# Optimization experiments

Measured on AMD Instinct MI355X. Metric: run time of the kernel, lower is better.

The kernel has to match this reference:

```python
import jax, jax.numpy as jnp
import numpy as np
from jax import lax

B, S, H, E, P, K, R = 64, 512, 768, 32, 16, 9, 6
HEADS, C1, C2 = 4, 128, 64
FEAT = 4 * C2 + 1  # e1, e2, e1*e2, context (64 each) + log-distance


def _ln(x, g, b):
    m = x.mean(-1, keepdims=True)
    v = ((x - m) ** 2).mean(-1, keepdims=True)
    return (x - m) * lax.rsqrt(v + 1e-5) * g + b


def _gat(x, adj, W, a_s, a_d, bias, heads, cout, concat):
    # Dense GATConv over a small fully-masked entity graph. adj[b,i,j]=edge j->i (incl. self-loops).
    h = jnp.einsum('bef,fhc->behc', x, W.reshape(x.shape[-1], heads, cout))
    s = jnp.einsum('behc,hc->bhe', h, a_s)  # source-node attention term
    d = jnp.einsum('behc,hc->bhe', h, a_d)  # target-node attention term
    logits = jax.nn.leaky_relu(d[:, :, :, None] + s[:, :, None, :], 0.2)  # [b,h,i,j]
    logits = jnp.where(adj[:, None, :, :], logits, -1e9)
    att = jax.nn.softmax(logits, axis=-1)
    out = jnp.einsum('bhij,bjhc->bihc', att, h)
    out = out.reshape(out.shape[0], out.shape[1], heads * cout) if concat else out.mean(2)
    return out + bias


def _crf_nll(em, tags, mask, start, end, trans):
    # torchcrf: loss = -mean log-likelihood. em [B,S,K]; tags [B,S]; mask [B,S] bool.
    emt = jnp.transpose(em, (1, 0, 2))
    tgt = tags.T
    mkt = mask.T.astype(em.dtype)
    num0 = start[tgt[0]] + jnp.take_along_axis(emt[0], tgt[0][:, None], 1)[:, 0]

    def nstep(c, inp):
        ptag, sc = c
        e, t, m = inp
        step = trans[ptag, t] + jnp.take_along_axis(e, t[:, None], 1)[:, 0]
        return (jnp.where(m > 0, t, ptag), sc + step * m), None

    (ltag, num), _ = lax.scan(nstep, (tgt[0], num0), (emt[1:], tgt[1:], mkt[1:]))
    num = num + end[ltag]
    a0 = start[None, :] + emt[0]

    def dstep(a, inp):
        e, m = inp
        nxt = jax.scipy.special.logsumexp(a[:, :, None] + trans[None] + e[:, None, :], axis=1)
        return jnp.where(m[:, None] > 0, nxt, a), None

    aT, _ = lax.scan(dstep, a0, (emt[1:], mkt[1:]))
    Z = jax.scipy.special.logsumexp(aT + end[None], axis=1)
    return jnp.mean(Z - num)


def setup_inputs() -> dict:
    key = jax.random.key(0)
    ks = jax.random.split(key, 24)
    n = lambda i, shape, s=0.05: jax.random.normal(ks[i], shape, jnp.float32) * s
    return {
        'sequence_output': jax.random.normal(ks[0], (B, S, H), jnp.float32),
        'attention_mask': jnp.ones((B, S), jnp.int32),
        'ner_labels': jax.random.randint(ks[1], (B, S), 0, K),
        'entity_start': jax.random.randint(ks[2], (B, E), 0, S - 8),
        'entity_len': jax.random.randint(ks[3], (B, E), 0, 8),
        'pair_e1': jax.random.randint(ks[4], (B, P), 0, E),
        'pair_e2': jax.random.randint(ks[5], (B, P), 0, E),
        'pair_labels': jax.random.randint(ks[6], (B, P), 0, 2),
        'adj_mask': jnp.ones((B, E, E), bool),
        'w_ner1': n(7, (H, 256)), 'b_ner1': jnp.zeros((256,), jnp.float32),
        'w_ner2': n(8, (256, K)), 'b_ner2': jnp.zeros((K,), jnp.float32),
        'crf_start': n(9, (K,), 0.1), 'crf_end': n(10, (K,), 0.1), 'crf_trans': n(11, (K, K), 0.1),
        'w_gat1': n(12, (H, HEADS * C1)), 'a_src1': n(13, (HEADS, C1)), 'a_dst1': n(14, (HEADS, C1)),
        'b_gat1': jnp.zeros((HEADS * C1,), jnp.float32),
        'w_gat2': n(15, (HEADS * C1, C2)), 'a_src2': n(16, (1, C2)), 'a_dst2': n(17, (1, C2)),
        'b_gat2': jnp.zeros((C2,), jnp.float32),
        'w_fe': n(18, (FEAT, 512)), 'b_fe': jnp.zeros((512,), jnp.float32),
        'g_fe': jnp.ones((512,), jnp.float32), 'be_fe': jnp.zeros((512,), jnp.float32),
        'w_rc1': n(19, (R, 512, 256)), 'b_rc1': jnp.zeros((R, 256), jnp.float32),
        'g_rc': jnp.ones((R, 256), jnp.float32), 'be_rc': jnp.zeros((R, 256), jnp.float32),
        'w_rc2': n(20, (R, 256, 1)), 'b_rc2': jnp.zeros((R,), jnp.float32),
    }


def reference(sequence_output, attention_mask, ner_labels, entity_start, entity_len,
              pair_e1, pair_e2, pair_labels, adj_mask,
              w_ner1, b_ner1, w_ner2, b_ner2, crf_start, crf_end, crf_trans,
              w_gat1, a_src1, a_dst1, b_gat1, w_gat2, a_src2, a_dst2, b_gat2,
              w_fe, b_fe, g_fe, be_fe, w_rc1, b_rc1, g_rc, be_rc, w_rc2, b_rc2):
    # NER head (dropout off / eval)
    ner_logits = jnp.maximum(sequence_output @ w_ner1 + b_ner1, 0.0) @ w_ner2 + b_ner2
    ner_loss = _crf_nll(ner_logits, ner_labels, attention_mask.astype(bool),
                        crf_start, crf_end, crf_trans)
    # entity span mean-pool via inclusive cumsum trick
    cs = jnp.concatenate([jnp.zeros((B, 1, H), sequence_output.dtype),
                          jnp.cumsum(sequence_output, axis=1)], axis=1)
    e_end = jnp.clip(entity_start + entity_len, 0, S - 1)
    seg = (jnp.take_along_axis(cs, (e_end + 1)[:, :, None], 1)
           - jnp.take_along_axis(cs, entity_start[:, :, None], 1))
    ent = seg / (e_end - entity_start + 1).astype(sequence_output.dtype)[:, :, None]  # [B,E,H]
    x = _gat(ent, adj_mask, w_gat1, a_src1, a_dst1, b_gat1, HEADS, C1, True)
    x = jnp.maximum(x, 0.0)
    x = _gat(x, adj_mask, w_gat2, a_src2, a_dst2, b_gat2, 1, C2, False)  # [B,E,64]
    x1 = jnp.take_along_axis(x, pair_e1[:, :, None], 1)
    x2 = jnp.take_along_axis(x, pair_e2[:, :, None], 1)
    ctx = jnp.broadcast_to(x.mean(1, keepdims=True), (B, P, C2))
    dist = jnp.log(jnp.abs(pair_e1 - pair_e2).astype(x.dtype) + 1.0)[:, :, None]
    pf = jnp.concatenate([x1, x2, x1 * x2, ctx, dist], axis=-1)  # [B,P,257]
    fe = jax.nn.leaky_relu(_ln(pf @ w_fe + b_fe, g_fe, be_fe), 0.01)
    h1 = jnp.einsum('bpf,rfo->rbpo', fe, w_rc1) + b_rc1[:, None, None, :]
    h1 = jax.nn.leaky_relu(_ln(h1, g_rc[:, None, None, :], be_rc[:, None, None, :]), 0.01)
    z = jnp.einsum('rbpo,ro->rbp', h1, w_rc2[:, :, 0]) + b_rc2[:, None, None]
    y = pair_labels.astype(z.dtype)[None]
    # BCEWithLogitsLoss(pos_weight=2.0), mean per relation type, summed over types
    bce = -(2.0 * y * jax.nn.log_sigmoid(z) + (1.0 - y) * jax.nn.log_sigmoid(-z))
    rel_loss = bce.mean(axis=(1, 2)).sum()
    total = ner_loss + rel_loss
    return ner_logits, z, total
```

## Files before the change

### kernel.cpp

```cpp
#include <hip/hip_runtime.h>
#include <math.h>


#define NB 64
#define NS 512
#define NH 768
#define NE 32
#define NP 16
#define NK 9
#define NR 6
#define NHEADS 4
#define NC1 128
#define NC2 64
#define SEGS 16
#define SEGLEN 32

#define ZOFF 294912
#define TOTOFF 301056

#define WS_ENT   0u
#define WS_HG1   1572864u
#define WS_X1    2621440u
#define WS_H2    3670016u
#define WS_X2    3801088u
#define WS_S1    3932160u
#define WS_D1    3940352u
#define WS_S2    3948544u
#define WS_D2    3950592u
#define WS_CTX   3952640u
#define WS_PF    3956736u
#define WS_FE    4222976u
#define WS_CRF   4747264u
#define WS_REL   4747328u
#define WS_W1T   4747392u
#define WS_WRT   0u
#define WS_WFET  393216u
#define WS_SEG   475136u

typedef __attribute__((ext_vector_type(8))) short bf16x8;
typedef __attribute__((ext_vector_type(4))) float f32x4;

__device__ __forceinline__ unsigned short f2bf(float x) {
  union { float f; unsigned u; } v; v.f = x;
  unsigned r = v.u + 0x7FFFu + ((v.u >> 16) & 1u);
  return (unsigned short)(r >> 16);
}

__device__ __forceinline__ float logsigf(float x) {
  if (x >= 0.f) return -log1pf(__expf(-x));
  return x - log1pf(__expf(x));
}

__global__ __launch_bounds__(256) void k_w1t(const float* __restrict__ w1,
    unsigned short* __restrict__ w1t) {
  const int k = blockIdx.x, t = threadIdx.x;
  w1t[t * NH + k] = f2bf(w1[k * 256 + t]);
}

__global__ __launch_bounds__(256) void k_wrt(const float* __restrict__ w1,
    unsigned short* __restrict__ wrt) {
  __shared__ unsigned short tr[256 * 72];
  const int r = blockIdx.x >> 3, kt = blockIdx.x & 7;
  const int k0 = kt * 64, t = threadIdx.x;
#pragma unroll
  for (int i = 0; i < 16; i++) {
    const int slot = t + 256 * i;
    const int row = slot >> 6, c4 = slot & 63;
    const float4 f = *reinterpret_cast<const float4*>(
        &w1[((size_t)(r * 512) + k0 + row) * 256 + c4 * 4]);
    tr[(c4 * 4 + 0) * 72 + row] = f2bf(f.x);
    tr[(c4 * 4 + 1) * 72 + row] = f2bf(f.y);
    tr[(c4 * 4 + 2) * 72 + row] = f2bf(f.z);
    tr[(c4 * 4 + 3) * 72 + row] = f2bf(f.w);
  }
  __syncthreads();
#pragma unroll
  for (int i = 0; i < 8; i++) {
    const int slot = t + 256 * i;
    const int col = slot >> 3, q = slot & 7;
    *reinterpret_cast<uint4*>(&wrt[((size_t)(r * 256 + col)) * 512 + k0 + q * 8]) =
        *reinterpret_cast<const uint4*>(&tr[col * 72 + q * 8]);
  }
}

__global__ __launch_bounds__(256) void k_wfet(const float* __restrict__ w,
    unsigned short* __restrict__ wt) {
  __shared__ unsigned short tr[256 * 72];
  const int kt = blockIdx.x % 5, cb = blockIdx.x / 5;
  const int k0 = kt * 64, c0 = cb * 256, t = threadIdx.x;
#pragma unroll
  for (int i = 0; i < 16; i++) {
    const int slot = t + 256 * i;
    const int row = slot >> 6, c4 = slot & 63;
    const int k = k0 + row;
    float4 f = {0.f, 0.f, 0.f, 0.f};
    if (k < 257)
      f = *reinterpret_cast<const float4*>(&w[(size_t)k * 512 + c0 + c4 * 4]);
    tr[(c4 * 4 + 0) * 72 + row] = f2bf(f.x);
    tr[(c4 * 4 + 1) * 72 + row] = f2bf(f.y);
    tr[(c4 * 4 + 2) * 72 + row] = f2bf(f.z);
    tr[(c4 * 4 + 3) * 72 + row] = f2bf(f.w);
  }
  __syncthreads();
#pragma unroll
  for (int i = 0; i < 8; i++) {
    const int slot = t + 256 * i;
    const int col = slot >> 3, q = slot & 7;
    *reinterpret_cast<uint4*>(&wt[((size_t)(c0 + col)) * 320 + k0 + q * 8]) =
        *reinterpret_cast<const uint4*>(&tr[col * 72 + q * 8]);
  }
}

__global__ __launch_bounds__(256) void k_ner(const float* __restrict__ seq,
    const unsigned short* __restrict__ w1t, const float* __restrict__ b1,
    const float* __restrict__ w2, const float* __restrict__ b2,
    float* __restrict__ out) {
  __shared__ unsigned short AsS[64 * 40];
  __shared__ unsigned short BsS[256 * 40];
  __shared__ float zs[64 * 4 * 12];
  const int t = threadIdx.x;
  const int tok0 = blockIdx.x * 64;
  const int w = t >> 6, lane = t & 63, quad = lane >> 4, l15 = lane & 15;

  f32x4 acc[4][4];
#pragma unroll
  for (int r = 0; r < 4; r++)
#pragma unroll
    for (int c = 0; c < 4; c++) acc[r][c] = (f32x4){0.f, 0.f, 0.f, 0.f};

  const int tokA = t >> 2, koffA = (t & 3) * 8;
  const float* aptr = seq + (size_t)(tok0 + tokA) * NH + koffA;

  for (int kt = 0; kt < NH; kt += 32) {
    __syncthreads();
    {
      const float4 f0 = *reinterpret_cast<const float4*>(aptr + kt);
      const float4 f1 = *reinterpret_cast<const float4*>(aptr + kt + 4);
      bf16x8 av;
      av[0] = (short)f2bf(f0.x); av[1] = (short)f2bf(f0.y);
      av[2] = (short)f2bf(f0.z); av[3] = (short)f2bf(f0.w);
      av[4] = (short)f2bf(f1.x); av[5] = (short)f2bf(f1.y);
      av[6] = (short)f2bf(f1.z); av[7] = (short)f2bf(f1.w);
      *reinterpret_cast<bf16x8*>(&AsS[tokA * 40 + koffA]) = av;
    }
#pragma unroll
    for (int i = 0; i < 4; i++) {
      const int q = t + 256 * i;
      const int col = q >> 2, koff = (q & 3) * 8;
      *reinterpret_cast<uint4*>(&BsS[col * 40 + koff]) =
          *reinterpret_cast<const uint4*>(&w1t[(size_t)col * NH + kt + koff]);
    }
    __syncthreads();
    bf16x8 a[4], b[4];
#pragma unroll
    for (int r = 0; r < 4; r++)
      a[r] = *reinterpret_cast<const bf16x8*>(&AsS[(r * 16 + l15) * 40 + quad * 8]);
#pragma unroll
    for (int c = 0; c < 4; c++)
      b[c] = *reinterpret_cast<const bf16x8*>(&BsS[(w * 64 + c * 16 + l15) * 40 + quad * 8]);
#pragma unroll
    for (int r = 0; r < 4; r++)
#pragma unroll
      for (int c = 0; c < 4; c++)
        acc[r][c] = __builtin_amdgcn_mfma_f32_16x16x32_bf16(a[r], b[c], acc[r][c], 0, 0, 0);
  }

  float b1v[4], w2v[4][NK];
#pragma unroll
  for (int c = 0; c < 4; c++) {
    const int col = w * 64 + c * 16 + l15;
    b1v[c] = b1[col];
#pragma unroll
    for (int cc = 0; cc < NK; cc++) w2v[c][cc] = w2[col * NK + cc];
  }
#pragma unroll
  for (int r = 0; r < 4; r++) {
#pragma unroll
    for (int reg = 0; reg < 4; reg++) {
      float p[NK];
#pragma unroll
      for (int cc = 0; cc < NK; cc++) p[cc] = 0.f;
#pragma unroll
      for (int c = 0; c < 4; c++) {
        const float h = fmaxf(acc[r][c][reg] + b1v[c], 0.f);
#pragma unroll
        for (int cc = 0; cc < NK; cc++) p[cc] = fmaf(h, w2v[c][cc], p[cc]);
      }
#pragma unroll
      for (int o = 1; o < 16; o <<= 1)
#pragma unroll
        for (int cc = 0; cc < NK; cc++) p[cc] += __shfl_xor(p[cc], o);
      if (l15 == 0) {
        const int tokr = r * 16 + quad * 4 + reg;
#pragma unroll
        for (int cc = 0; cc < NK; cc++) zs[(tokr * 4 + w) * 12 + cc] = p[cc];
      }
    }
  }
  __syncthreads();
  if (t < 64) {
#pragma unroll
    for (int cc = 0; cc < NK; cc++) {
      const float z = zs[(t * 4 + 0) * 12 + cc] + zs[(t * 4 + 1) * 12 + cc] +
                      zs[(t * 4 + 2) * 12 + cc] + zs[(t * 4 + 3) * 12 + cc] + b2[cc];
      out[(size_t)(tok0 + t) * NK + cc] = z;
    }
  }
}

__global__ __launch_bounds__(128) void k_crf_seg(const float* __restrict__ em,
    const int* __restrict__ mask, const float* __restrict__ trans,
    float* __restrict__ segm) {
  __shared__ float bufA[16 * 81];
  __shared__ float bufB[8 * 81];
  __shared__ float ems[SEGLEN * 9];
  __shared__ int mks[SEGLEN];
  __shared__ float trs[81];
  const int blk = blockIdx.x;
  const int b = blk >> 4, seg = blk & 15;
  const int t = threadIdx.x;
  const int s0 = 1 + seg * SEGLEN;
  const float* emb = em + (size_t)b * NS * NK;
  const int* mk = mask + b * NS;
  if (t < 81) trs[t] = trans[t];
  for (int i = t; i < SEGLEN * 9; i += 128) {
    const int g = s0 * 9 + i;
    ems[i] = (g < NS * 9) ? emb[g] : 0.f;
  }
  if (t < SEGLEN) {
    const int s = s0 + t;
    mks[t] = (s < NS) ? mk[s] : 0;
  }
  __syncthreads();
  for (int idx = t; idx < 16 * 81; idx += 128) {
    const int p = idx / 81, e = idx % 81, i = e / 9, j = e % 9;
    const int la = 2 * p, lb = la + 1;
    const bool ma = mks[la] > 0, mb = mks[lb] > 0;
    float r;
    if (ma && mb) {
      float v[9], mx = -1e30f;
#pragma unroll
      for (int m = 0; m < 9; m++) {
        v[m] = trs[i * 9 + m] + ems[la * 9 + m] + trs[m * 9 + j];
        mx = fmaxf(mx, v[m]);
      }
      float sum = 0.f;
#pragma unroll
      for (int m = 0; m < 9; m++) sum += __expf(v[m] - mx);
      r = mx + __logf(sum) + ems[lb * 9 + j];
    } else if (ma) {
      r = trs[e] + ems[la * 9 + j];
    } else if (mb) {
      r = trs[e] + ems[lb * 9 + j];
    } else {
      r = (i == j) ? 0.f : -1e30f;
    }
    bufA[p * 81 + e] = r;
  }
  float* src = bufA;
  float* dst = bufB;
  for (int n = 16; n > 1; n >>= 1) {
    __syncthreads();
    const int half = n >> 1;
    for (int idx = t; idx < half * 81; idx += 128) {
      const int q = idx / 81, e = idx % 81, i = e / 9, j = e % 9;
      const float* A = src + (size_t)(2 * q) * 81;
      const float* Bm = src + (size_t)(2 * q + 1) * 81;
      float v[9], mx = -1e30f;
#pragma unroll
      for (int m = 0; m < 9; m++) {
        v[m] = A[i * 9 + m] + Bm[m * 9 + j];
        mx = fmaxf(mx, v[m]);
      }
      float sum = 0.f;
#pragma unroll
      for (int m = 0; m < 9; m++) sum += __expf(v[m] - mx);
      dst[q * 81 + e] = mx + __logf(sum);
    }
    float* tmp = src; src = dst; dst = tmp;
  }
  __syncthreads();
  if (t < 81) segm[((size_t)b * SEGS + seg) * 81 + t] = src[t];
}

__global__ __launch_bounds__(64) void k_crf_fin(const float* __restrict__ em,
    const int* __restrict__ tags, const int* __restrict__ mask,
    const float* __restrict__ startv, const float* __restrict__ endv,
    const float* __restrict__ trans, const float* __restrict__ segm,
    float* __restrict__ lossb) {
  __shared__ float sm[SEGS * 81];
  __shared__ float av[16];
  __shared__ float red[2];
  const int b = blockIdx.x, t = threadIdx.x;
  const float* emb = em + (size_t)b * NS * NK;
  const int* mk = mask + b * NS;
  const int* tg = tags + b * NS;
  for (int i = t; i < SEGS * 81; i += 64) sm[i] = segm[(size_t)b * SEGS * 81 + i];
  {
    float num = 0.f;
    int lastS = 0;
#pragma unroll
    for (int o = 0; o < 8; o++) {
      const int s = t * 8 + o;
      if (s >= 1 && mk[s] > 0) {
        const int cur = tg[s], prv = tg[s - 1];
        num += trans[prv * NK + cur] + emb[s * NK + cur];
        lastS = s;
      }
    }
#pragma unroll
    for (int o = 32; o > 0; o >>= 1) {
      num += __shfl_xor(num, o);
      lastS = max(lastS, __shfl_xor(lastS, o));
    }
    if (t == 0) {
      const int t0 = tg[0];
      red[0] = startv[t0] + emb[t0] + num + endv[tg[lastS]];
    }
  }
  __syncthreads();
  if (t < 9) av[t] = startv[t] + emb[t];
  __syncthreads();
  for (int h = 0; h < SEGS; h++) {
    float nv = 0.f;
    if (t < 9) {
      float v[9], mx = -1e30f;
#pragma unroll
      for (int i2 = 0; i2 < 9; i2++) {
        v[i2] = av[i2] + sm[h * 81 + i2 * 9 + t];
        mx = fmaxf(mx, v[i2]);
      }
      float sum = 0.f;
#pragma unroll
      for (int i2 = 0; i2 < 9; i2++) sum += __expf(v[i2] - mx);
      nv = mx + __logf(sum);
    }
    __syncthreads();
    if (t < 9) av[t] = nv;
    __syncthreads();
  }
  if (t == 0) {
    float mx = -1e30f;
#pragma unroll
    for (int j = 0; j < 9; j++) mx = fmaxf(mx, av[j] + endv[j]);
    float sum = 0.f;
#pragma unroll
    for (int j = 0; j < 9; j++) sum += __expf(av[j] + endv[j] - mx);
    lossb[b] = (mx + __logf(sum)) - red[0];
  }
}

__global__ __launch_bounds__(256) void k_ent(const float* __restrict__ seq,
    const int* __restrict__ est, const int* __restrict__ elen, float* __restrict__ ent) {
  const int be = blockIdx.x;
  const int b = be >> 5, e = be & 31;
  const int st = est[b * NE + e];
  int en = st + elen[b * NE + e];
  en = min(max(en, 0), NS - 1);
  const float inv = 1.f / (float)(en - st + 1);
  for (int c = threadIdx.x; c < NH; c += 256) {
    float s = 0.f;
    for (int r = st; r <= en; r++) s += seq[((size_t)b * NS + r) * NH + c];
    ent[((size_t)b * NE + e) * NH + c] = s * inv;
  }
}

__global__ __launch_bounds__(256) void k_g1(const float* __restrict__ ent,
    const float* __restrict__ w, float* __restrict__ hout) {
  __shared__ float As[32 * 36];
  __shared__ float Bs[32 * 128];
  const int b = blockIdx.x >> 2, cb = blockIdx.x & 3;
  const int t = threadIdx.x;
  const int tc = t & 31, tr = t >> 5;
  float acc[4][4];
#pragma unroll
  for (int i = 0; i < 4; i++)
#pragma unroll
    for (int j = 0; j < 4; j++) acc[i][j] = 0.f;
  for (int kt = 0; kt < NH; kt += 32) {
    __syncthreads();
    {
      const int e = t >> 3, k4 = t & 7;
      *reinterpret_cast<float4*>(&As[e * 36 + k4 * 4]) =
          *reinterpret_cast<const float4*>(&ent[((size_t)b * NE + e) * NH + kt + k4 * 4]);
    }
#pragma unroll
    for (int i = 0; i < 4; i++) {
      const int slot = t + 256 * i;
      const int row = slot >> 5, cg = slot & 31;
      *reinterpret_cast<float4*>(&Bs[row * 128 + cg * 4]) =
          *reinterpret_cast<const float4*>(&w[(size_t)(kt + row) * 512 + cb * 128 + cg * 4]);
    }
    __syncthreads();
#pragma unroll
    for (int kg = 0; kg < 8; kg++) {
      float4 a[4];
#pragma unroll
      for (int i = 0; i < 4; i++)
        a[i] = *reinterpret_cast<const float4*>(&As[(tr * 4 + i) * 36 + kg * 4]);
#pragma unroll
      for (int k2 = 0; k2 < 4; k2++) {
        const float4 bv = *reinterpret_cast<const float4*>(&Bs[(kg * 4 + k2) * 128 + tc * 4]);
#pragma unroll
        for (int i = 0; i < 4; i++) {
          const float av = reinterpret_cast<const float*>(&a[i])[k2];
          acc[i][0] = fmaf(av, bv.x, acc[i][0]);
          acc[i][1] = fmaf(av, bv.y, acc[i][1]);
          acc[i][2] = fmaf(av, bv.z, acc[i][2]);
          acc[i][3] = fmaf(av, bv.w, acc[i][3]);
        }
      }
    }
  }
#pragma unroll
  for (int i = 0; i < 4; i++) {
    float4 v;
    v.x = acc[i][0]; v.y = acc[i][1]; v.z = acc[i][2]; v.w = acc[i][3];
    *reinterpret_cast<float4*>(&hout[((size_t)b * NE + tr * 4 + i) * 512 + cb * 128 + tc * 4]) = v;
  }
}

__global__ __launch_bounds__(128) void k_sd1(const float* __restrict__ h,
    const float* __restrict__ as, const float* __restrict__ ad,
    float* __restrict__ s1, float* __restrict__ d1) {
  __shared__ float sm[4];
  const int be = blockIdx.x;
  const int b = be >> 5, e = be & 31;
  const int t = threadIdx.x;
  for (int hd = 0; hd < NHEADS; hd++) {
    const float v = h[((size_t)b * NE + e) * 512 + hd * NC1 + t];
    float sv = v * as[hd * NC1 + t];
    float dv = v * ad[hd * NC1 + t];
#pragma unroll
    for (int o = 32; o > 0; o >>= 1) { sv += __shfl_xor(sv, o); dv += __shfl_xor(dv, o); }
    if ((t & 63) == 0) { sm[(t >> 6) * 2] = sv; sm[(t >> 6) * 2 + 1] = dv; }
    __syncthreads();
    if (t == 0) {
      s1[(b * NHEADS + hd) * NE + e] = sm[0] + sm[2];
      d1[(b * NHEADS + hd) * NE + e] = sm[1] + sm[3];
    }
    __syncthreads();
  }
}

__global__ __launch_bounds__(128) void k_att1(const float* __restrict__ h,
    const float* __restrict__ s1, const float* __restrict__ d1,
    const unsigned char* __restrict__ adj, const float* __restrict__ bias,
    float* __restrict__ x1) {
  __shared__ float att[NE];
  const int blk = blockIdx.x;
  const int i = blk & 31, hd = (blk >> 5) & 3, b = blk >> 7;
  const int t = threadIdx.x;
  if (t < NE) {
    float lg = d1[(b * NHEADS + hd) * NE + i] + s1[(b * NHEADS + hd) * NE + t];
    lg = lg >= 0.f ? lg : 0.2f * lg;
    if (!adj[((size_t)b * NE + i) * NE + t]) lg = -1e9f;
    att[t] = lg;
  }
  __syncthreads();
  if (t == 0) {
    float m = -1e30f;
#pragma unroll
    for (int j = 0; j < NE; j++) m = fmaxf(m, att[j]);
    float ex[NE];
    float sum = 0.f;
#pragma unroll
    for (int j = 0; j < NE; j++) { ex[j] = __expf(att[j] - m); sum += ex[j]; }
    const float inv = 1.f / sum;
#pragma unroll
    for (int j = 0; j < NE; j++) att[j] = ex[j] * inv;
  }
  __syncthreads();
  float acc = bias[hd * NC1 + t];
  for (int j = 0; j < NE; j++)
    acc += att[j] * h[((size_t)b * NE + j) * 512 + hd * NC1 + t];
  x1[((size_t)b * NE + i) * 512 + hd * NC1 + t] = fmaxf(acc, 0.f);
}

__global__ __launch_bounds__(256) void k_g2(const float* __restrict__ x1,
    const float* __restrict__ w, const float* __restrict__ as, const float* __restrict__ ad,
    float* __restrict__ h2, float* __restrict__ s2, float* __restrict__ d2) {
  __shared__ float As[32 * 36];
  __shared__ float Bs[32 * 64];
  const int b = blockIdx.x;
  const int t = threadIdx.x;
  const int tc = t & 15, tr = t >> 4;
  float acc[2][4];
#pragma unroll
  for (int i = 0; i < 2; i++)
#pragma unroll
    for (int j = 0; j < 4; j++) acc[i][j] = 0.f;
  for (int kt = 0; kt < 512; kt += 32) {
    __syncthreads();
    {
      const int e = t >> 3, k4 = t & 7;
      *reinterpret_cast<float4*>(&As[e * 36 + k4 * 4]) =
          *reinterpret_cast<const float4*>(&x1[((size_t)b * NE + e) * 512 + kt + k4 * 4]);
    }
#pragma unroll
    for (int i = 0; i < 2; i++) {
      const int slot = t + 256 * i;
      const int row = slot >> 4, cg = slot & 15;
      *reinterpret_cast<float4*>(&Bs[row * 64 + cg * 4]) =
          *reinterpret_cast<const float4*>(&w[(size_t)(kt + row) * NC2 + cg * 4]);
    }
    __syncthreads();
#pragma unroll
    for (int kg = 0; kg < 8; kg++) {
      float4 a[2];
#pragma unroll
      for (int i = 0; i < 2; i++)
        a[i] = *reinterpret_cast<const float4*>(&As[(tr * 2 + i) * 36 + kg * 4]);
#pragma unroll
      for (int k2 = 0; k2 < 4; k2++) {
        const float4 bv = *reinterpret_cast<const float4*>(&Bs[(kg * 4 + k2) * 64 + tc * 4]);
#pragma unroll
        for (int i = 0; i < 2; i++) {
          const float av = reinterpret_cast<const float*>(&a[i])[k2];
          acc[i][0] = fmaf(av, bv.x, acc[i][0]);
          acc[i][1] = fmaf(av, bv.y, acc[i][1]);
          acc[i][2] = fmaf(av, bv.z, acc[i][2]);
          acc[i][3] = fmaf(av, bv.w, acc[i][3]);
        }
      }
    }
  }
  const float4 a4s = *reinterpret_cast<const float4*>(&as[tc * 4]);
  const float4 a4d = *reinterpret_cast<const float4*>(&ad[tc * 4]);
#pragma unroll
  for (int i = 0; i < 2; i++) {
    const int e = tr * 2 + i;
    float4 v;
    v.x = acc[i][0]; v.y = acc[i][1]; v.z = acc[i][2]; v.w = acc[i][3];
    *reinterpret_cast<float4*>(&h2[((size_t)b * NE + e) * NC2 + tc * 4]) = v;
    float sv = v.x * a4s.x + v.y * a4s.y + v.z * a4s.z + v.w * a4s.w;
    float dv = v.x * a4d.x + v.y * a4d.y + v.z * a4d.z + v.w * a4d.w;
#pragma unroll
    for (int o = 8; o > 0; o >>= 1) { sv += __shfl_xor(sv, o); dv += __shfl_xor(dv, o); }
    if (tc == 0) { s2[b * NE + e] = sv; d2[b * NE + e] = dv; }
  }
}

__global__ __launch_bounds__(64) void k_att2(const float* __restrict__ h2,
    const float* __restrict__ s2, const float* __restrict__ d2,
    const unsigned char* __restrict__ adj, const float* __restrict__ bias,
    float* __restrict__ x2) {
  __shared__ float att[NE];
  const int be = blockIdx.x;
  const int b = be >> 5, i = be & 31;
  const int t = threadIdx.x;
  if (t < NE) {
    float lg = d2[b * NE + i] + s2[b * NE + t];
    lg = lg >= 0.f ? lg : 0.2f * lg;
    if (!adj[((size_t)b * NE + i) * NE + t]) lg = -1e9f;
    att[t] = lg;
  }
  __syncthreads();
  if (t == 0) {
    float m = -1e30f;
#pragma unroll
    for (int j = 0; j < NE; j++) m = fmaxf(m, att[j]);
    float ex[NE];
    float sum = 0.f;
#pragma unroll
    for (int j = 0; j < NE; j++) { ex[j] = __expf(att[j] - m); sum += ex[j]; }
    const float inv = 1.f / sum;
#pragma unroll
    for (int j = 0; j < NE; j++) att[j] = ex[j] * inv;
  }
  __syncthreads();
  float acc = bias[t];
  for (int j = 0; j < NE; j++)
    acc += att[j] * h2[((size_t)b * NE + j) * NC2 + t];
  x2[((size_t)b * NE + i) * NC2 + t] = acc;
}

__global__ __launch_bounds__(64) void k_ctx(const float* __restrict__ x2, float* __restrict__ ctx) {
  const int b = blockIdx.x, t = threadIdx.x;
  float s = 0.f;
  for (int e = 0; e < NE; e++) s += x2[((size_t)b * NE + e) * NC2 + t];
  ctx[b * NC2 + t] = s * (1.f / NE);
}

__global__ __launch_bounds__(64) void k_pf(const float* __restrict__ x2,
    const float* __restrict__ ctx, const int* __restrict__ pe1, const int* __restrict__ pe2,
    float* __restrict__ pf) {
  const int bp = blockIdx.x;
  const int b = bp >> 4, p = bp & 15;
  const int t = threadIdx.x;
  const int e1 = pe1[b * NP + p], e2 = pe2[b * NP + p];
  const float v1 = x2[((size_t)b * NE + e1) * NC2 + t];
  const float v2 = x2[((size_t)b * NE + e2) * NC2 + t];
  float* row = pf + (size_t)bp * 260;
  row[t] = v1;
  row[64 + t] = v2;
  row[128 + t] = v1 * v2;
  row[192 + t] = ctx[b * NC2 + t];
  if (t == 0) row[256] = logf(fabsf((float)(e1 - e2)) + 1.f);
  if (t < 3) row[257 + t] = 0.f;
}

__global__ __launch_bounds__(256) void k_fe(const float* __restrict__ pf,
    const unsigned short* __restrict__ wt, const float* __restrict__ bfe,
    const float* __restrict__ g, const float* __restrict__ be,
    unsigned short* __restrict__ feb) {
  __shared__ unsigned short Af[16 * 320];
  __shared__ float Cs[16 * 520];
  const int b = blockIdx.x, t = threadIdx.x;
  const int w = t >> 6, lane = t & 63, quad = lane >> 4, l15 = lane & 15;
  for (int i = t; i < 16 * 320; i += 256) {
    const int p = i / 320, k = i - p * 320;
    Af[i] = (k < 260) ? f2bf(pf[(size_t)(b * NP + p) * 260 + k]) : (unsigned short)0;
  }
  __syncthreads();
  f32x4 acc[8];
#pragma unroll
  for (int c = 0; c < 8; c++) acc[c] = (f32x4){0.f, 0.f, 0.f, 0.f};
#pragma unroll
  for (int kt = 0; kt < 10; kt++) {
    const bf16x8 a = *reinterpret_cast<const bf16x8*>(&Af[l15 * 320 + kt * 32 + quad * 8]);
#pragma unroll
    for (int c = 0; c < 8; c++) {
      const int col = w * 128 + c * 16 + l15;
      const bf16x8 bv = *reinterpret_cast<const bf16x8*>(&wt[(size_t)col * 320 + kt * 32 + quad * 8]);
      acc[c] = __builtin_amdgcn_mfma_f32_16x16x32_bf16(a, bv, acc[c], 0, 0, 0);
    }
  }
#pragma unroll
  for (int c = 0; c < 8; c++)
#pragma unroll
    for (int reg = 0; reg < 4; reg++)
      Cs[(quad * 4 + reg) * 520 + w * 128 + c * 16 + l15] = acc[c][reg];
  __syncthreads();
  float bfev[8], gv[8], bev[8];
#pragma unroll
  for (int ch = 0; ch < 8; ch++) {
    const int col = ch * 64 + lane;
    bfev[ch] = bfe[col]; gv[ch] = g[col]; bev[ch] = be[col];
  }
#pragma unroll
  for (int pp = 0; pp < 4; pp++) {
    const int p = w * 4 + pp;
    float v[8], s = 0.f, sq = 0.f;
#pragma unroll
    for (int ch = 0; ch < 8; ch++) {
      v[ch] = Cs[p * 520 + ch * 64 + lane] + bfev[ch];
      s += v[ch]; sq += v[ch] * v[ch];
    }
#pragma unroll
    for (int o = 32; o > 0; o >>= 1) { s += __shfl_xor(s, o); sq += __shfl_xor(sq, o); }
    const float mean = s * (1.f / 512.f);
    const float var = sq * (1.f / 512.f) - mean * mean;
    const float rr = rsqrtf(var + 1e-5f);
#pragma unroll
    for (int ch = 0; ch < 8; ch++) {
      float n = (v[ch] - mean) * rr * gv[ch] + bev[ch];
      n = n >= 0.f ? n : 0.01f * n;
      feb[(size_t)(b * NP + p) * 512 + ch * 64 + lane] = f2bf(n);
    }
  }
}

__global__ __launch_bounds__(256) void k_rc(const unsigned short* __restrict__ feb,
    const unsigned short* __restrict__ wrt, const float* __restrict__ b1,
    const float* __restrict__ g, const float* __restrict__ be,
    const float* __restrict__ w2, const float* __restrict__ b2,
    const int* __restrict__ ylab, float* __restrict__ zout, float* __restrict__ relacc) {
  __shared__ unsigned short Af[16 * 520];
  __shared__ float Cs[16 * 264];
  const int blk = blockIdx.x;
  const int r = blk >> 6, b = blk & 63;
  const int t = threadIdx.x;
  const int w = t >> 6, lane = t & 63, quad = lane >> 4, l15 = lane & 15;
#pragma unroll
  for (int i = 0; i < 4; i++) {
    const int slot = t + 256 * i;
    const int p = slot >> 6, q = slot & 63;
    *reinterpret_cast<uint4*>(&Af[p * 520 + q * 8]) =
        *reinterpret_cast<const uint4*>(&feb[(size_t)(b * NP + p) * 512 + q * 8]);
  }
  __syncthreads();
  f32x4 acc[4];
#pragma unroll
  for (int c = 0; c < 4; c++) acc[c] = (f32x4){0.f, 0.f, 0.f, 0.f};
#pragma unroll
  for (int kt = 0; kt < 16; kt++) {
    const bf16x8 a = *reinterpret_cast<const bf16x8*>(&Af[l15 * 520 + kt * 32 + quad * 8]);
#pragma unroll
    for (int c = 0; c < 4; c++) {
      const int col = w * 64 + c * 16 + l15;
      const bf16x8 bv = *reinterpret_cast<const bf16x8*>(
          &wrt[(size_t)(r * 256 + col) * 512 + kt * 32 + quad * 8]);
      acc[c] = __builtin_amdgcn_mfma_f32_16x16x32_bf16(a, bv, acc[c], 0, 0, 0);
    }
  }
#pragma unroll
  for (int c = 0; c < 4; c++)
#pragma unroll
    for (int reg = 0; reg < 4; reg++)
      Cs[(quad * 4 + reg) * 264 + w * 64 + c * 16 + l15] = acc[c][reg];
  __syncthreads();
  float b1v[4], gv[4], bev[4], w2v[4];
#pragma unroll
  for (int ch = 0; ch < 4; ch++) {
    const int col = r * 256 + ch * 64 + lane;
    b1v[ch] = b1[col]; gv[ch] = g[col]; bev[ch] = be[col]; w2v[ch] = w2[col];
  }
  const float b2v = b2[r];
  float local = 0.f;
#pragma unroll
  for (int pp = 0; pp < 4; pp++) {
    const int p = w * 4 + pp;
    float v[4], s = 0.f, sq = 0.f;
#pragma unroll
    for (int ch = 0; ch < 4; ch++) {
      v[ch] = Cs[p * 264 + ch * 64 + lane] + b1v[ch];
      s += v[ch]; sq += v[ch] * v[ch];
    }
#pragma unroll
    for (int o = 32; o > 0; o >>= 1) { s += __shfl_xor(s, o); sq += __shfl_xor(sq, o); }
    const float mean = s * (1.f / 256.f);
    const float var = sq * (1.f / 256.f) - mean * mean;
    const float rr = rsqrtf(var + 1e-5f);
    float zdot = 0.f;
#pragma unroll
    for (int ch = 0; ch < 4; ch++) {
      float n = (v[ch] - mean) * rr * gv[ch] + bev[ch];
      n = n >= 0.f ? n : 0.01f * n;
      zdot = fmaf(n, w2v[ch], zdot);
    }
#pragma unroll
    for (int o = 32; o > 0; o >>= 1) zdot += __shfl_xor(zdot, o);
    if (lane == 0) {
      const float zp = zdot + b2v;
      zout[(size_t)(r * NB + b) * NP + p] = zp;
      const float y = (float)ylab[b * NP + p];
      local += -(2.f * y * logsigf(zp) + (1.f - y) * logsigf(-zp));
    }
  }
  if (lane == 0) atomicAdd(relacc, local * (1.f / (NB * NP)));
}

__global__ __launch_bounds__(64) void k_fin(const float* __restrict__ lossb,
    const float* __restrict__ rel, float* __restrict__ out) {
  float v = lossb[threadIdx.x];
#pragma unroll
  for (int o = 32; o > 0; o >>= 1) v += __shfl_down(v, o);
  if (threadIdx.x == 0) out[TOTOFF] = v * (1.f / NB) + rel[0];
}

extern "C" void kernel_launch(void* const* d_in, const int* in_sizes, int n_in,
                              void* d_out, int out_size, void* d_ws, size_t ws_size,
                              hipStream_t stream) {
  const float* seq = (const float*)d_in[0];
  const int* amask = (const int*)d_in[1];
  const int* nlab = (const int*)d_in[2];
  const int* est = (const int*)d_in[3];
  const int* elen = (const int*)d_in[4];
  const int* pe1 = (const int*)d_in[5];
  const int* pe2 = (const int*)d_in[6];
  const int* plab = (const int*)d_in[7];
  const unsigned char* adj = (const unsigned char*)d_in[8];
  const float* w_ner1 = (const float*)d_in[9];
  const float* b_ner1 = (const float*)d_in[10];
  const float* w_ner2 = (const float*)d_in[11];
  const float* b_ner2 = (const float*)d_in[12];
  const float* crf_start = (const float*)d_in[13];
  const float* crf_end = (const float*)d_in[14];
  const float* crf_trans = (const float*)d_in[15];
  const float* w_gat1 = (const float*)d_in[16];
  const float* a_src1 = (const float*)d_in[17];
  const float* a_dst1 = (const float*)d_in[18];
  const float* b_gat1 = (const float*)d_in[19];
  const float* w_gat2 = (const float*)d_in[20];
  const float* a_src2 = (const float*)d_in[21];
  const float* a_dst2 = (const float*)d_in[22];
  const float* b_gat2 = (const float*)d_in[23];
  const float* w_fe = (const float*)d_in[24];
  const float* b_fe = (const float*)d_in[25];
  const float* g_fe = (const float*)d_in[26];
  const float* be_fe = (const float*)d_in[27];
  const float* w_rc1 = (const float*)d_in[28];
  const float* b_rc1 = (const float*)d_in[29];
  const float* g_rc = (const float*)d_in[30];
  const float* be_rc = (const float*)d_in[31];
  const float* w_rc2 = (const float*)d_in[32];
  const float* b_rc2 = (const float*)d_in[33];

  float* out = (float*)d_out;
  float* ws = (float*)d_ws;
  float* ent = ws + WS_ENT;
  float* hg1 = ws + WS_HG1;
  float* x1 = ws + WS_X1;
  float* h2 = ws + WS_H2;
  float* x2 = ws + WS_X2;
  float* s1 = ws + WS_S1;
  float* d1 = ws + WS_D1;
  float* s2 = ws + WS_S2;
  float* d2 = ws + WS_D2;
  float* ctx = ws + WS_CTX;
  float* pf = ws + WS_PF;
  float* crfb = ws + WS_CRF;
  float* rel = ws + WS_REL;
  unsigned short* w1t = (unsigned short*)(ws + WS_W1T);
  unsigned short* feb = (unsigned short*)(ws + WS_FE);
  unsigned short* wrt = (unsigned short*)(ws + WS_WRT);
  unsigned short* wfet = (unsigned short*)(ws + WS_WFET);
  float* segm = ws + WS_SEG;

  hipMemsetAsync(rel, 0, sizeof(float), stream);

  k_w1t<<<NH, 256, 0, stream>>>(w_ner1, w1t);
  k_ner<<<512, 256, 0, stream>>>(seq, w1t, b_ner1, w_ner2, b_ner2, out);
  k_ent<<<NB * NE, 256, 0, stream>>>(seq, est, elen, ent);
  k_g1<<<NB * 4, 256, 0, stream>>>(ent, w_gat1, hg1);
  k_wrt<<<NR * 8, 256, 0, stream>>>(w_rc1, wrt);
  k_wfet<<<10, 256, 0, stream>>>(w_fe, wfet);
  k_crf_seg<<<NB * SEGS, 128, 0, stream>>>(out, amask, crf_trans, segm);
  k_crf_fin<<<NB, 64, 0, stream>>>(out, nlab, amask, crf_start, crf_end, crf_trans,
                                   segm, crfb);
  k_sd1<<<NB * NE, 128, 0, stream>>>(hg1, a_src1, a_dst1, s1, d1);
  k_att1<<<NB * NHEADS * NE, 128, 0, stream>>>(hg1, s1, d1, adj, b_gat1, x1);
  k_g2<<<NB, 256, 0, stream>>>(x1, w_gat2, a_src2, a_dst2, h2, s2, d2);
  k_att2<<<NB * NE, 64, 0, stream>>>(h2, s2, d2, adj, b_gat2, x2);
  k_ctx<<<NB, 64, 0, stream>>>(x2, ctx);
  k_pf<<<NB * NP, 64, 0, stream>>>(x2, ctx, pe1, pe2, pf);
  k_fe<<<NB, 256, 0, stream>>>(pf, wfet, b_fe, g_fe, be_fe, feb);
  k_rc<<<NR * NB, 256, 0, stream>>>(feb, wrt, b_rc1, g_rc, be_rc, w_rc2, b_rc2,
                                    plab, out + ZOFF, rel);
  k_fin<<<1, 64, 0, stream>>>(crfb, rel, out);
}
```

Measured before the change: 444.1 us.

## Fuse GAT projection, attention scores, softmax and aggregation into per-head kernels

Merges the GAT layer-1 projection with the src/dst score computation, softmax and neighbor aggregation into one kernel per (batch, head), doing the same for layer 2. The context mean is folded into the pair-feature kernel, and the two weight-conversion kernels are merged into one launch. The NER weight transpose now goes through shared memory with coalesced vector stores. This removes several launches and the global round-trips of intermediate h, s, d and ctx buffers. In exchange, the pair kernel redundantly recomputes the entity mean for each pair, and a single warp per block does the softmax.

```diff
diff --git a/kernel.cpp b/kernel.cpp
--- a/kernel.cpp
+++ b/kernel.cpp
@@ -19,15 +19,8 @@
 #define TOTOFF 301056
 
 #define WS_ENT   0u
-#define WS_HG1   1572864u
 #define WS_X1    2621440u
-#define WS_H2    3670016u
 #define WS_X2    3801088u
-#define WS_S1    3932160u
-#define WS_D1    3940352u
-#define WS_S2    3948544u
-#define WS_D2    3950592u
-#define WS_CTX   3952640u
 #define WS_PF    3956736u
 #define WS_FE    4222976u
 #define WS_CRF   4747264u
@@ -53,61 +46,79 @@
 
 __global__ __launch_bounds__(256) void k_w1t(const float* __restrict__ w1,
     unsigned short* __restrict__ w1t) {
-  const int k = blockIdx.x, t = threadIdx.x;
-  w1t[t * NH + k] = f2bf(w1[k * 256 + t]);
-}
-
-__global__ __launch_bounds__(256) void k_wrt(const float* __restrict__ w1,
-    unsigned short* __restrict__ wrt) {
+  __shared__ unsigned short tr[32 * 776];
+  const int c0 = blockIdx.x * 32;
+  const int t = threadIdx.x;
+#pragma unroll
+  for (int p = 0; p < 24; p++) {
+    const int k = p * 32 + (t >> 3), c4 = t & 7;
+    const float4 f = *reinterpret_cast<const float4*>(&w1[(size_t)k * 256 + c0 + c4 * 4]);
+    tr[(c4 * 4 + 0) * 776 + k] = f2bf(f.x);
+    tr[(c4 * 4 + 1) * 776 + k] = f2bf(f.y);
+    tr[(c4 * 4 + 2) * 776 + k] = f2bf(f.z);
+    tr[(c4 * 4 + 3) * 776 + k] = f2bf(f.w);
+  }
+  __syncthreads();
+  const int c = t >> 3, q = t & 7;
+#pragma unroll
+  for (int i = 0; i < 12; i++) {
+    *reinterpret_cast<uint4*>(&w1t[(size_t)(c0 + c) * NH + q * 96 + i * 8]) =
+        *reinterpret_cast<const uint4*>(&tr[c * 776 + q * 96 + i * 8]);
+  }
+}
+
+__global__ __launch_bounds__(256) void k_wconv(const float* __restrict__ wrc,
+    const float* __restrict__ wfe, unsigned short* __restrict__ wrt,
+    unsigned short* __restrict__ wfet) {
   __shared__ unsigned short tr[256 * 72];
-  const int r = blockIdx.x >> 3, kt = blockIdx.x & 7;
-  const int k0 = kt * 64, t = threadIdx.x;
-#pragma unroll
-  for (int i = 0; i < 16; i++) {
-    const int slot = t + 256 * i;
-    const int row = slot >> 6, c4 = slot & 63;
-    const float4 f = *reinterpret_cast<const float4*>(
-        &w1[((size_t)(r * 512) + k0 + row) * 256 + c4 * 4]);
-    tr[(c4 * 4 + 0) * 72 + row] = f2bf(f.x);
-    tr[(c4 * 4 + 1) * 72 + row] = f2bf(f.y);
-    tr[(c4 * 4 + 2) * 72 + row] = f2bf(f.z);
-    tr[(c4 * 4 + 3) * 72 + row] = f2bf(f.w);
-  }
-  __syncthreads();
-#pragma unroll
-  for (int i = 0; i < 8; i++) {
-    const int slot = t + 256 * i;
-    const int col = slot >> 3, q = slot & 7;
-    *reinterpret_cast<uint4*>(&wrt[((size_t)(r * 256 + col)) * 512 + k0 + q * 8]) =
-        *reinterpret_cast<const uint4*>(&tr[col * 72 + q * 8]);
-  }
-}
-
-__global__ __launch_bounds__(256) void k_wfet(const float* __restrict__ w,
-    unsigned short* __restrict__ wt) {
-  __shared__ unsigned short tr[256 * 72];
-  const int kt = blockIdx.x % 5, cb = blockIdx.x / 5;
-  const int k0 = kt * 64, c0 = cb * 256, t = threadIdx.x;
-#pragma unroll
-  for (int i = 0; i < 16; i++) {
-    const int slot = t + 256 * i;
-    const int row = slot >> 6, c4 = slot & 63;
-    const int k = k0 + row;
-    float4 f = {0.f, 0.f, 0.f, 0.f};
-    if (k < 257)
-      f = *reinterpret_cast<const float4*>(&w[(size_t)k * 512 + c0 + c4 * 4]);
-    tr[(c4 * 4 + 0) * 72 + row] = f2bf(f.x);
-    tr[(c4 * 4 + 1) * 72 + row] = f2bf(f.y);
-    tr[(c4 * 4 + 2) * 72 + row] = f2bf(f.z);
-    tr[(c4 * 4 + 3) * 72 + row] = f2bf(f.w);
-  }
-  __syncthreads();
-#pragma unroll
-  for (int i = 0; i < 8; i++) {
-    const int slot = t + 256 * i;
-    const int col = slot >> 3, q = slot & 7;
-    *reinterpret_cast<uint4*>(&wt[((size_t)(c0 + col)) * 320 + k0 + q * 8]) =
-        *reinterpret_cast<const uint4*>(&tr[col * 72 + q * 8]);
+  const int t = threadIdx.x;
+  if (blockIdx.x < 48) {
+    const int r = blockIdx.x >> 3, kt = blockIdx.x & 7;
+    const int k0 = kt * 64;
+#pragma unroll
+    for (int i = 0; i < 16; i++) {
+      const int slot = t + 256 * i;
+      const int row = slot >> 6, c4 = slot & 63;
+      const float4 f = *reinterpret_cast<const float4*>(
+          &wrc[((size_t)(r * 512) + k0 + row) * 256 + c4 * 4]);
+      tr[(c4 * 4 + 0) * 72 + row] = f2bf(f.x);
+      tr[(c4 * 4 + 1) * 72 + row] = f2bf(f.y);
+      tr[(c4 * 4 + 2) * 72 + row] = f2bf(f.z);
+      tr[(c4 * 4 + 3) * 72 + row] = f2bf(f.w);
+    }
+    __syncthreads();
+#pragma unroll
+    for (int i = 0; i < 8; i++) {
+      const int slot = t + 256 * i;
+      const int col = slot >> 3, q = slot & 7;
+      *reinterpret_cast<uint4*>(&wrt[((size_t)(r * 256 + col)) * 512 + k0 + q * 8]) =
+          *reinterpret_cast<const uint4*>(&tr[col * 72 + q * 8]);
+    }
+  } else {
+    const int bid = blockIdx.x - 48;
+    const int kt = bid % 5, cb = bid / 5;
+    const int k0 = kt * 64, c0 = cb * 256;
+#pragma unroll
+    for (int i = 0; i < 16; i++) {
+      const int slot = t + 256 * i;
+      const int row = slot >> 6, c4 = slot & 63;
+      const int k = k0 + row;
+      float4 f = {0.f, 0.f, 0.f, 0.f};
+      if (k < 257)
+        f = *reinterpret_cast<const float4*>(&wfe[(size_t)k * 512 + c0 + c4 * 4]);
+      tr[(c4 * 4 + 0) * 72 + row] = f2bf(f.x);
+      tr[(c4 * 4 + 1) * 72 + row] = f2bf(f.y);
+      tr[(c4 * 4 + 2) * 72 + row] = f2bf(f.z);
+      tr[(c4 * 4 + 3) * 72 + row] = f2bf(f.w);
+    }
+    __syncthreads();
+#pragma unroll
+    for (int i = 0; i < 8; i++) {
+      const int slot = t + 256 * i;
+      const int col = slot >> 3, q = slot & 7;
+      *reinterpret_cast<uint4*>(&wfet[((size_t)(c0 + col)) * 320 + k0 + q * 8]) =
+          *reinterpret_cast<const uint4*>(&tr[col * 72 + q * 8]);
+    }
   }
 }
 
@@ -365,11 +376,16 @@
   }
 }
 
-__global__ __launch_bounds__(256) void k_g1(const float* __restrict__ ent,
-    const float* __restrict__ w, float* __restrict__ hout) {
+__global__ __launch_bounds__(256) void k_g1f(const float* __restrict__ ent,
+    const float* __restrict__ w, const float* __restrict__ as,
+    const float* __restrict__ ad, const unsigned char* __restrict__ adj,
+    const float* __restrict__ bias, float* __restrict__ x1) {
   __shared__ float As[32 * 36];
   __shared__ float Bs[32 * 128];
-  const int b = blockIdx.x >> 2, cb = blockIdx.x & 3;
+  __shared__ float Hs[32 * 132];
+  __shared__ float Att[32 * 32];
+  __shared__ float Sv[32], Dv[32];
+  const int b = blockIdx.x >> 2, hd = blockIdx.x & 3;
   const int t = threadIdx.x;
   const int tc = t & 31, tr = t >> 5;
   float acc[4][4];
@@ -389,7 +405,7 @@
       const int slot = t + 256 * i;
       const int row = slot >> 5, cg = slot & 31;
       *reinterpret_cast<float4*>(&Bs[row * 128 + cg * 4]) =
-          *reinterpret_cast<const float4*>(&w[(size_t)(kt + row) * 512 + cb * 128 + cg * 4]);
+          *reinterpret_cast<const float4*>(&w[(size_t)(kt + row) * 512 + hd * 128 + cg * 4]);
     }
     __syncthreads();
 #pragma unroll
@@ -413,75 +429,76 @@
     }
   }
 #pragma unroll
+  for (int i = 0; i < 4; i++)
+#pragma unroll
+    for (int j = 0; j < 4; j++)
+      Hs[(tr * 4 + i) * 132 + tc * 4 + j] = acc[i][j];
+  __syncthreads();
+  {
+    const int e = t >> 3, cg = t & 7;
+    float sv = 0.f, dv = 0.f;
+#pragma unroll
+    for (int c = 0; c < 16; c++) {
+      const float h = Hs[e * 132 + cg * 16 + c];
+      sv += h * as[hd * NC1 + cg * 16 + c];
+      dv += h * ad[hd * NC1 + cg * 16 + c];
+    }
+#pragma unroll
+    for (int o = 1; o < 8; o <<= 1) { sv += __shfl_xor(sv, o); dv += __shfl_xor(dv, o); }
+    if (cg == 0) { Sv[e] = sv; Dv[e] = dv; }
+  }
+  __syncthreads();
+  if (t < 32) {
+    const int i = t;
+    const float di = Dv[i];
+    float lg[32];
+    float m = -1e30f;
+#pragma unroll
+    for (int j = 0; j < 32; j++) {
+      float v = di + Sv[j];
+      v = v >= 0.f ? v : 0.2f * v;
+      if (!adj[((size_t)b * NE + i) * NE + j]) v = -1e9f;
+      lg[j] = v; m = fmaxf(m, v);
+    }
+    float sum = 0.f;
+#pragma unroll
+    for (int j = 0; j < 32; j++) { lg[j] = __expf(lg[j] - m); sum += lg[j]; }
+    const float inv = 1.f / sum;
+#pragma unroll
+    for (int j = 0; j < 32; j++) Att[j * 32 + i] = lg[j] * inv;
+  }
+  __syncthreads();
+#pragma unroll
   for (int i = 0; i < 4; i++) {
+    const int row = tr * 4 + i;
+    float o0 = bias[hd * NC1 + tc * 4 + 0];
+    float o1 = bias[hd * NC1 + tc * 4 + 1];
+    float o2 = bias[hd * NC1 + tc * 4 + 2];
+    float o3 = bias[hd * NC1 + tc * 4 + 3];
+#pragma unroll
+    for (int j = 0; j < 32; j++) {
+      const float a = Att[j * 32 + row];
+      o0 = fmaf(a, Hs[j * 132 + tc * 4 + 0], o0);
+      o1 = fmaf(a, Hs[j * 132 + tc * 4 + 1], o1);
+      o2 = fmaf(a, Hs[j * 132 + tc * 4 + 2], o2);
+      o3 = fmaf(a, Hs[j * 132 + tc * 4 + 3], o3);
+    }
     float4 v;
-    v.x = acc[i][0]; v.y = acc[i][1]; v.z = acc[i][2]; v.w = acc[i][3];
-    *reinterpret_cast<float4*>(&hout[((size_t)b * NE + tr * 4 + i) * 512 + cb * 128 + tc * 4]) = v;
-  }
-}
-
-__global__ __launch_bounds__(128) void k_sd1(const float* __restrict__ h,
-    const float* __restrict__ as, const float* __restrict__ ad,
-    float* __restrict__ s1, float* __restrict__ d1) {
-  __shared__ float sm[4];
-  const int be = blockIdx.x;
-  const int b = be >> 5, e = be & 31;
-  const int t = threadIdx.x;
-  for (int hd = 0; hd < NHEADS; hd++) {
-    const float v = h[((size_t)b * NE + e) * 512 + hd * NC1 + t];
-    float sv = v * as[hd * NC1 + t];
-    float dv = v * ad[hd * NC1 + t];
-#pragma unroll
-    for (int o = 32; o > 0; o >>= 1) { sv += __shfl_xor(sv, o); dv += __shfl_xor(dv, o); }
-    if ((t & 63) == 0) { sm[(t >> 6) * 2] = sv; sm[(t >> 6) * 2 + 1] = dv; }
-    __syncthreads();
-    if (t == 0) {
-      s1[(b * NHEADS + hd) * NE + e] = sm[0] + sm[2];
-      d1[(b * NHEADS + hd) * NE + e] = sm[1] + sm[3];
-    }
-    __syncthreads();
-  }
-}
-
-__global__ __launch_bounds__(128) void k_att1(const float* __restrict__ h,
-    const float* __restrict__ s1, const float* __restrict__ d1,
-    const unsigned char* __restrict__ adj, const float* __restrict__ bias,
-    float* __restrict__ x1) {
-  __shared__ float att[NE];
-  const int blk = blockIdx.x;
-  const int i = blk & 31, hd = (blk >> 5) & 3, b = blk >> 7;
-  const int t = threadIdx.x;
-  if (t < NE) {
-    float lg = d1[(b * NHEADS + hd) * NE + i] + s1[(b * NHEADS + hd) * NE + t];
-    lg = lg >= 0.f ? lg : 0.2f * lg;
-    if (!adj[((size_t)b * NE + i) * NE + t]) lg = -1e9f;
-    att[t] = lg;
-  }
-  __syncthreads();
-  if (t == 0) {
-    float m = -1e30f;
-#pragma unroll
-    for (int j = 0; j < NE; j++) m = fmaxf(m, att[j]);
-    float ex[NE];
-    float sum = 0.f;
-#pragma unroll
-    for (int j = 0; j < NE; j++) { ex[j] = __expf(att[j] - m); sum += ex[j]; }
-    const float inv = 1.f / sum;
-#pragma unroll
-    for (int j = 0; j < NE; j++) att[j] = ex[j] * inv;
-  }
-  __syncthreads();
-  float acc = bias[hd * NC1 + t];
-  for (int j = 0; j < NE; j++)
-    acc += att[j] * h[((size_t)b * NE + j) * 512 + hd * NC1 + t];
-  x1[((size_t)b * NE + i) * 512 + hd * NC1 + t] = fmaxf(acc, 0.f);
-}
-
-__global__ __launch_bounds__(256) void k_g2(const float* __restrict__ x1,
-    const float* __restrict__ w, const float* __restrict__ as, const float* __restrict__ ad,
-    float* __restrict__ h2, float* __restrict__ s2, float* __restrict__ d2) {
+    v.x = fmaxf(o0, 0.f); v.y = fmaxf(o1, 0.f);
+    v.z = fmaxf(o2, 0.f); v.w = fmaxf(o3, 0.f);
+    *reinterpret_cast<float4*>(&x1[((size_t)b * NE + row) * 512 + hd * 128 + tc * 4]) = v;
+  }
+}
+
+__global__ __launch_bounds__(256) void k_g2f(const float* __restrict__ x1,
+    const float* __restrict__ w, const float* __restrict__ as,
+    const float* __restrict__ ad, const unsigned char* __restrict__ adj,
+    const float* __restrict__ bias, float* __restrict__ x2) {
   __shared__ float As[32 * 36];
   __shared__ float Bs[32 * 64];
+  __shared__ float H2[32 * 68];
+  __shared__ float Att[32 * 32];
+  __shared__ float Sv[32], Dv[32];
   const int b = blockIdx.x;
   const int t = threadIdx.x;
   const int tc = t & 15, tr = t >> 4;
@@ -532,58 +549,57 @@
     const int e = tr * 2 + i;
     float4 v;
     v.x = acc[i][0]; v.y = acc[i][1]; v.z = acc[i][2]; v.w = acc[i][3];
-    *reinterpret_cast<float4*>(&h2[((size_t)b * NE + e) * NC2 + tc * 4]) = v;
+    *reinterpret_cast<float4*>(&H2[e * 68 + tc * 4]) = v;
     float sv = v.x * a4s.x + v.y * a4s.y + v.z * a4s.z + v.w * a4s.w;
     float dv = v.x * a4d.x + v.y * a4d.y + v.z * a4d.z + v.w * a4d.w;
 #pragma unroll
     for (int o = 8; o > 0; o >>= 1) { sv += __shfl_xor(sv, o); dv += __shfl_xor(dv, o); }
-    if (tc == 0) { s2[b * NE + e] = sv; d2[b * NE + e] = dv; }
-  }
-}
-
-__global__ __launch_bounds__(64) void k_att2(const float* __restrict__ h2,
-    const float* __restrict__ s2, const float* __restrict__ d2,
-    const unsigned char* __restrict__ adj, const float* __restrict__ bias,
-    float* __restrict__ x2) {
-  __shared__ float att[NE];
-  const int be = blockIdx.x;
-  const int b = be >> 5, i = be & 31;
-  const int t = threadIdx.x;
-  if (t < NE) {
-    float lg = d2[b * NE + i] + s2[b * NE + t];
-    lg = lg >= 0.f ? lg : 0.2f * lg;
-    if (!adj[((size_t)b * NE + i) * NE + t]) lg = -1e9f;
-    att[t] = lg;
-  }
-  __syncthreads();
-  if (t == 0) {
+    if (tc == 0) { Sv[e] = sv; Dv[e] = dv; }
+  }
+  __syncthreads();
+  if (t < 32) {
+    const int i = t;
+    const float di = Dv[i];
+    float lg[32];
     float m = -1e30f;
 #pragma unroll
-    for (int j = 0; j < NE; j++) m = fmaxf(m, att[j]);
-    float ex[NE];
+    for (int j = 0; j < 32; j++) {
+      float v = di + Sv[j];
+      v = v >= 0.f ? v : 0.2f * v;
+      if (!adj[((size_t)b * NE + i) * NE + j]) v = -1e9f;
+      lg[j] = v; m = fmaxf(m, v);
+    }
     float sum = 0.f;
 #pragma unroll
-    for (int j = 0; j < NE; j++) { ex[j] = __expf(att[j] - m); sum += ex[j]; }
+    for (int j = 0; j < 32; j++) { lg[j] = __expf(lg[j] - m); sum += lg[j]; }
     const float inv = 1.f / sum;
 #pragma unroll
-    for (int j = 0; j < NE; j++) att[j] = ex[j] * inv;
-  }
-  __syncthreads();
-  float acc = bias[t];
-  for (int j = 0; j < NE; j++)
-    acc += att[j] * h2[((size_t)b * NE + j) * NC2 + t];
-  x2[((size_t)b * NE + i) * NC2 + t] = acc;
-}
-
-__global__ __launch_bounds__(64) void k_ctx(const float* __restrict__ x2, float* __restrict__ ctx) {
-  const int b = blockIdx.x, t = threadIdx.x;
-  float s = 0.f;
-  for (int e = 0; e < NE; e++) s += x2[((size_t)b * NE + e) * NC2 + t];
-  ctx[b * NC2 + t] = s * (1.f / NE);
+    for (int j = 0; j < 32; j++) Att[j * 32 + i] = lg[j] * inv;
+  }
+  __syncthreads();
+#pragma unroll
+  for (int i = 0; i < 2; i++) {
+    const int row = tr * 2 + i;
+    float o0 = bias[tc * 4 + 0];
+    float o1 = bias[tc * 4 + 1];
+    float o2 = bias[tc * 4 + 2];
+    float o3 = bias[tc * 4 + 3];
+#pragma unroll
+    for (int j = 0; j < 32; j++) {
+      const float a = Att[j * 32 + row];
+      o0 = fmaf(a, H2[j * 68 + tc * 4 + 0], o0);
+      o1 = fmaf(a, H2[j * 68 + tc * 4 + 1], o1);
+      o2 = fmaf(a, H2[j * 68 + tc * 4 + 2], o2);
+      o3 = fmaf(a, H2[j * 68 + tc * 4 + 3], o3);
+    }
+    float4 v;
+    v.x = o0; v.y = o1; v.z = o2; v.w = o3;
+    *reinterpret_cast<float4*>(&x2[((size_t)b * NE + row) * NC2 + tc * 4]) = v;
+  }
 }
 
 __global__ __launch_bounds__(64) void k_pf(const float* __restrict__ x2,
-    const float* __restrict__ ctx, const int* __restrict__ pe1, const int* __restrict__ pe2,
+    const int* __restrict__ pe1, const int* __restrict__ pe2,
     float* __restrict__ pf) {
   const int bp = blockIdx.x;
   const int b = bp >> 4, p = bp & 15;
@@ -591,11 +607,13 @@
   const int e1 = pe1[b * NP + p], e2 = pe2[b * NP + p];
   const float v1 = x2[((size_t)b * NE + e1) * NC2 + t];
   const float v2 = x2[((size_t)b * NE + e2) * NC2 + t];
+  float cs = 0.f;
+  for (int e = 0; e < NE; e++) cs += x2[((size_t)b * NE + e) * NC2 + t];
   float* row = pf + (size_t)bp * 260;
   row[t] = v1;
   row[64 + t] = v2;
   row[128 + t] = v1 * v2;
-  row[192 + t] = ctx[b * NC2 + t];
+  row[192 + t] = cs * (1.f / NE);
   if (t == 0) row[256] = logf(fabsf((float)(e1 - e2)) + 1.f);
   if (t < 3) row[257 + t] = 0.f;
 }
@@ -790,15 +808,8 @@
   float* out = (float*)d_out;
   float* ws = (float*)d_ws;
   float* ent = ws + WS_ENT;
-  float* hg1 = ws + WS_HG1;
   float* x1 = ws + WS_X1;
-  float* h2 = ws + WS_H2;
   float* x2 = ws + WS_X2;
-  float* s1 = ws + WS_S1;
-  float* d1 = ws + WS_D1;
-  float* s2 = ws + WS_S2;
-  float* d2 = ws + WS_D2;
-  float* ctx = ws + WS_CTX;
   float* pf = ws + WS_PF;
   float* crfb = ws + WS_CRF;
   float* rel = ws + WS_REL;
@@ -810,21 +821,16 @@
 
   hipMemsetAsync(rel, 0, sizeof(float), stream);
 
-  k_w1t<<<NH, 256, 0, stream>>>(w_ner1, w1t);
+  k_w1t<<<8, 256, 0, stream>>>(w_ner1, w1t);
   k_ner<<<512, 256, 0, stream>>>(seq, w1t, b_ner1, w_ner2, b_ner2, out);
   k_ent<<<NB * NE, 256, 0, stream>>>(seq, est, elen, ent);
-  k_g1<<<NB * 4, 256, 0, stream>>>(ent, w_gat1, hg1);
-  k_wrt<<<NR * 8, 256, 0, stream>>>(w_rc1, wrt);
-  k_wfet<<<10, 256, 0, stream>>>(w_fe, wfet);
+  k_g1f<<<NB * NHEADS, 256, 0, stream>>>(ent, w_gat1, a_src1, a_dst1, adj, b_gat1, x1);
+  k_wconv<<<58, 256, 0, stream>>>(w_rc1, w_fe, wrt, wfet);
   k_crf_seg<<<NB * SEGS, 128, 0, stream>>>(out, amask, crf_trans, segm);
   k_crf_fin<<<NB, 64, 0, stream>>>(out, nlab, amask, crf_start, crf_end, crf_trans,
                                    segm, crfb);
-  k_sd1<<<NB * NE, 128, 0, stream>>>(hg1, a_src1, a_dst1, s1, d1);
-  k_att1<<<NB * NHEADS * NE, 128, 0, stream>>>(hg1, s1, d1, adj, b_gat1, x1);
-  k_g2<<<NB, 256, 0, stream>>>(x1, w_gat2, a_src2, a_dst2, h2, s2, d2);
-  k_att2<<<NB * NE, 64, 0, stream>>>(h2, s2, d2, adj, b_gat2, x2);
-  k_ctx<<<NB, 64, 0, stream>>>(x2, ctx);
-  k_pf<<<NB * NP, 64, 0, stream>>>(x2, ctx, pe1, pe2, pf);
+  k_g2f<<<NB, 256, 0, stream>>>(x1, w_gat2, a_src2, a_dst2, adj, b_gat2, x2);
+  k_pf<<<NB * NP, 64, 0, stream>>>(x2, pe1, pe2, pf);
   k_fe<<<NB, 256, 0, stream>>>(pf, wfet, b_fe, g_fe, be_fe, feb);
   k_rc<<<NR * NB, 256, 0, stream>>>(feb, wrt, b_rc1, g_rc, be_rc, w_rc2, b_rc2,
                                     plab, out + ZOFF, rel);
```

Result: slower. 472.4 us (+6.4%).
